# Optimization experiments

Hardware: AMD Instinct MI355X
Metric: run time of the kernel (lower is better)

Reference implementation:

```python
import jax, jax.numpy as jnp
import numpy as np

K = 9          # kernel_size (search window)
PAD = 4        # padding = (K-1)//2

def setup_inputs() -> dict:
    key = jax.random.key(0)
    k1, k2 = jax.random.split(key)
    B, C, H, W = 16, 512, 38, 68
    feat1 = jax.random.normal(k1, (B, C, H, W), dtype=jnp.float32)
    feat2 = jax.random.normal(k2, (B, C, H, W), dtype=jnp.float32)
    return {"feat1": feat1, "feat2": feat2}

def reference(feat1, feat2):
    # corr[b,c,k,h,w] = feat1[b,c,h,w] * feat2_pad[b,c,h+dy,w+dx]; output = max over the
    # K*K window offsets k. We compute the max incrementally over the 81 fixed offsets
    # instead of materializing the [B,C,81,H,W] unfold tensor (same math, less memory).
    B, C, H, W = feat1.shape
    f2 = jnp.pad(feat2, ((0, 0), (0, 0), (PAD, PAD), (PAD, PAD)))
    out = None
    for dy in range(K):
        for dx in range(K):
            corr = feat1 * f2[:, :, dy:dy + H, dx:dx + W]  # [B,C,H,W]
            out = corr if out is None else jnp.maximum(out, corr)
    return out
```

## Files before the change

kernel.cpp:

```cpp
#include <hip/hip_runtime.h>


#define BB 16
#define CC 512
#define HH 38
#define WW 68
#define PLANE (HH * WW)
#define S2S 84
#define HMROWS 48

__global__ __launch_bounds__(256) void corr_winmax_kernel(
    const float* __restrict__ f1, const float* __restrict__ f2,
    float* __restrict__ out)
{
    __shared__ float  s2[HH * S2S];
    __shared__ float2 hm[HMROWS * WW];

    const int t = threadIdx.x;
    const int base = blockIdx.x * PLANE;

    for (int i = t; i < 456; i += 256) {
        int r = i / 12, j = i % 12;
        int col = (j < 4) ? j : (j + 68);
        s2[r * S2S + col] = 0.0f;
    }
    for (int i = t; i < 680; i += 256) {
        int rr = i / 68, col = i % 68;
        int row = (rr < 4) ? rr : (rr + 38);
        hm[row * WW + col] = make_float2(0.0f, 0.0f);
    }
    for (int j = t; j < 646; j += 256) {
        int r = j / 17, q = j % 17;
        float4 v = *reinterpret_cast<const float4*>(f2 + base + r * WW + q * 4);
        *reinterpret_cast<float4*>(&s2[r * S2S + 4 + q * 4]) = v;
    }
    __syncthreads();

    for (int j = t; j < 304; j += 256) {
        int r = j >> 3, seg = j & 7, c0 = seg * 9;
        float v[17];
        #pragma unroll
        for (int i = 0; i < 17; ++i) v[i] = s2[r * S2S + c0 + i];
        float ax[16], an[16];
        #pragma unroll
        for (int i = 0; i < 16; ++i) { ax[i] = fmaxf(v[i], v[i+1]); an[i] = fminf(v[i], v[i+1]); }
        float bx[14], bn[14];
        #pragma unroll
        for (int i = 0; i < 14; ++i) { bx[i] = fmaxf(ax[i], ax[i+2]); bn[i] = fminf(an[i], an[i+2]); }
        float cx[10], cn[10];
        #pragma unroll
        for (int i = 0; i < 10; ++i) { cx[i] = fmaxf(bx[i], bx[i+4]); cn[i] = fminf(bn[i], bn[i+4]); }
        #pragma unroll
        for (int k = 0; k < 9; ++k) {
            int col = c0 + k;
            if (col < WW)
                hm[(r + 4) * WW + col] =
                    make_float2(fmaxf(cx[k], v[k+8]), fminf(cn[k], v[k+8]));
        }
    }
    __syncthreads();

    for (int j = t; j < 272; j += 256) {
        int col = j % 68, vs = j / 68, h0 = vs * 10;
        float2 u[18];
        #pragma unroll
        for (int i = 0; i < 18; ++i) u[i] = hm[(h0 + i) * WW + col];
        float ax[17], an[17];
        #pragma unroll
        for (int i = 0; i < 17; ++i) { ax[i] = fmaxf(u[i].x, u[i+1].x); an[i] = fminf(u[i].y, u[i+1].y); }
        float bx[15], bn[15];
        #pragma unroll
        for (int i = 0; i < 15; ++i) { bx[i] = fmaxf(ax[i], ax[i+2]); bn[i] = fminf(an[i], an[i+2]); }
        float cx[11], cn[11];
        #pragma unroll
        for (int i = 0; i < 11; ++i) { cx[i] = fmaxf(bx[i], bx[i+4]); cn[i] = fminf(bn[i], bn[i+4]); }
        #pragma unroll
        for (int k = 0; k < 10; ++k) {
            int h = h0 + k;
            if (h < HH) {
                float mx = fmaxf(cx[k], u[k+8].x);
                float mn = fminf(cn[k], u[k+8].y);
                int idx = base + h * WW + col;
                float a = f1[idx];
                out[idx] = a * (a >= 0.0f ? mx : mn);
            }
        }
    }
}

extern "C" void kernel_launch(void* const* d_in, const int* in_sizes, int n_in,
                              void* d_out, int out_size, void* d_ws, size_t ws_size,
                              hipStream_t stream) {
    const float* f1 = (const float*)d_in[0];
    const float* f2 = (const float*)d_in[1];
    float* out = (float*)d_out;
    corr_winmax_kernel<<<dim3(BB * CC), dim3(256), 0, stream>>>(f1, f2, out);
}
```

Measured before the change: 51.25 us.

## Split max/min passes to shrink shared memory and raise occupancy

The separable window max/min is restructured into two sequential passes, max then min, that share a single float horizontal buffer instead of a float2 buffer. The staging copy of feat2 into shared memory is dropped, and feat2 is read straight from global with boundary checks. Blocks grow to 320 threads with a launch bound of 8 blocks per CU, and the vertical pass handles two columns per thread with float2 loads and stores. This cuts shared memory and register pressure to allow more resident blocks, at the cost of reading feat2 from global twice, an extra barrier pair, and poorly coalesced scalar global loads.

Result: slower. 75.01 us (+46.4%).

```diff
diff --git a/kernel.cpp b/kernel.cpp
--- a/kernel.cpp
+++ b/kernel.cpp
@@ -1,89 +1,125 @@
 #include <hip/hip_runtime.h>
 
 
-#define BB 16
-#define CC 512
 #define HH 38
 #define WW 68
 #define PLANE (HH * WW)
-#define S2S 84
-#define HMROWS 48
+#define NB (16 * 512)
+#define HBR 46
+#define TPB 320
 
-__global__ __launch_bounds__(256) void corr_winmax_kernel(
+__global__ __launch_bounds__(TPB, 8) void corr_sep_kernel(
     const float* __restrict__ f1, const float* __restrict__ f2,
     float* __restrict__ out)
 {
-    __shared__ float  s2[HH * S2S];
-    __shared__ float2 hm[HMROWS * WW];
+    __shared__ float hbuf[HBR * WW];
+    __shared__ float vmax[HH * WW];
 
     const int t = threadIdx.x;
     const int base = blockIdx.x * PLANE;
+    const float* __restrict__ f2p = f2 + base;
 
-    for (int i = t; i < 456; i += 256) {
-        int r = i / 12, j = i % 12;
-        int col = (j < 4) ? j : (j + 68);
-        s2[r * S2S + col] = 0.0f;
+    for (int i = t; i < 136; i += TPB) {
+        int rr = i / 17, q = i % 17;
+        int row = (rr < 4) ? rr : rr + HH;
+        *reinterpret_cast<float4*>(&hbuf[row * WW + q * 4]) = make_float4(0, 0, 0, 0);
     }
-    for (int i = t; i < 680; i += 256) {
-        int rr = i / 68, col = i % 68;
-        int row = (rr < 4) ? rr : (rr + 38);
-        hm[row * WW + col] = make_float2(0.0f, 0.0f);
-    }
-    for (int j = t; j < 646; j += 256) {
-        int r = j / 17, q = j % 17;
-        float4 v = *reinterpret_cast<const float4*>(f2 + base + r * WW + q * 4);
-        *reinterpret_cast<float4*>(&s2[r * S2S + 4 + q * 4]) = v;
-    }
-    __syncthreads();
 
-    for (int j = t; j < 304; j += 256) {
-        int r = j >> 3, seg = j & 7, c0 = seg * 9;
+    if (t < 304) {
+        int r = t >> 3, seg = t & 7, c0 = seg * 9;
         float v[17];
         #pragma unroll
-        for (int i = 0; i < 17; ++i) v[i] = s2[r * S2S + c0 + i];
-        float ax[16], an[16];
+        for (int i = 0; i < 17; ++i) {
+            int cc = c0 - 4 + i;
+            v[i] = (cc >= 0 && cc < WW) ? f2p[r * WW + cc] : 0.0f;
+        }
+        float d1[16], d2[14], d4[10];
         #pragma unroll
-        for (int i = 0; i < 16; ++i) { ax[i] = fmaxf(v[i], v[i+1]); an[i] = fminf(v[i], v[i+1]); }
-        float bx[14], bn[14];
+        for (int i = 0; i < 16; ++i) d1[i] = fmaxf(v[i], v[i + 1]);
         #pragma unroll
-        for (int i = 0; i < 14; ++i) { bx[i] = fmaxf(ax[i], ax[i+2]); bn[i] = fminf(an[i], an[i+2]); }
-        float cx[10], cn[10];
+        for (int i = 0; i < 14; ++i) d2[i] = fmaxf(d1[i], d1[i + 2]);
         #pragma unroll
-        for (int i = 0; i < 10; ++i) { cx[i] = fmaxf(bx[i], bx[i+4]); cn[i] = fminf(bn[i], bn[i+4]); }
+        for (int i = 0; i < 10; ++i) d4[i] = fmaxf(d2[i], d2[i + 4]);
         #pragma unroll
         for (int k = 0; k < 9; ++k) {
             int col = c0 + k;
-            if (col < WW)
-                hm[(r + 4) * WW + col] =
-                    make_float2(fmaxf(cx[k], v[k+8]), fminf(cn[k], v[k+8]));
+            if (col < WW) hbuf[(r + 4) * WW + col] = fmaxf(d4[k], v[k + 8]);
         }
     }
     __syncthreads();
 
-    for (int j = t; j < 272; j += 256) {
-        int col = j % 68, vs = j / 68, h0 = vs * 10;
+    if (t < 136) {
+        int cp = t % 34, vs = t / 34;
+        int c2 = cp * 2;
+        int h0 = (vs == 3) ? 28 : vs * 10;
         float2 u[18];
         #pragma unroll
-        for (int i = 0; i < 18; ++i) u[i] = hm[(h0 + i) * WW + col];
-        float ax[17], an[17];
+        for (int i = 0; i < 18; ++i)
+            u[i] = *reinterpret_cast<const float2*>(&hbuf[(h0 + i) * WW + c2]);
+        float2 d1[17], d2[15], d4[10];
         #pragma unroll
-        for (int i = 0; i < 17; ++i) { ax[i] = fmaxf(u[i].x, u[i+1].x); an[i] = fminf(u[i].y, u[i+1].y); }
-        float bx[15], bn[15];
+        for (int i = 0; i < 17; ++i) d1[i] = make_float2(fmaxf(u[i].x, u[i+1].x), fmaxf(u[i].y, u[i+1].y));
         #pragma unroll
-        for (int i = 0; i < 15; ++i) { bx[i] = fmaxf(ax[i], ax[i+2]); bn[i] = fminf(an[i], an[i+2]); }
-        float cx[11], cn[11];
+        for (int i = 0; i < 15; ++i) d2[i] = make_float2(fmaxf(d1[i].x, d1[i+2].x), fmaxf(d1[i].y, d1[i+2].y));
         #pragma unroll
-        for (int i = 0; i < 11; ++i) { cx[i] = fmaxf(bx[i], bx[i+4]); cn[i] = fminf(bn[i], bn[i+4]); }
+        for (int i = 0; i < 10; ++i) d4[i] = make_float2(fmaxf(d2[i].x, d2[i+4].x), fmaxf(d2[i].y, d2[i+4].y));
         #pragma unroll
         for (int k = 0; k < 10; ++k) {
             int h = h0 + k;
-            if (h < HH) {
-                float mx = fmaxf(cx[k], u[k+8].x);
-                float mn = fminf(cn[k], u[k+8].y);
-                int idx = base + h * WW + col;
-                float a = f1[idx];
-                out[idx] = a * (a >= 0.0f ? mx : mn);
-            }
+            float2 m = make_float2(fmaxf(d4[k].x, u[k+8].x), fmaxf(d4[k].y, u[k+8].y));
+            *reinterpret_cast<float2*>(&vmax[h * WW + c2]) = m;
+        }
+    }
+    __syncthreads();
+
+    if (t < 304) {
+        int r = t >> 3, seg = t & 7, c0 = seg * 9;
+        float v[17];
+        #pragma unroll
+        for (int i = 0; i < 17; ++i) {
+            int cc = c0 - 4 + i;
+            v[i] = (cc >= 0 && cc < WW) ? f2p[r * WW + cc] : 0.0f;
+        }
+        float d1[16], d2[14], d4[10];
+        #pragma unroll
+        for (int i = 0; i < 16; ++i) d1[i] = fminf(v[i], v[i + 1]);
+        #pragma unroll
+        for (int i = 0; i < 14; ++i) d2[i] = fminf(d1[i], d1[i + 2]);
+        #pragma unroll
+        for (int i = 0; i < 10; ++i) d4[i] = fminf(d2[i], d2[i + 4]);
+        #pragma unroll
+        for (int k = 0; k < 9; ++k) {
+            int col = c0 + k;
+            if (col < WW) hbuf[(r + 4) * WW + col] = fminf(d4[k], v[k + 8]);
+        }
+    }
+    __syncthreads();
+
+    if (t < 136) {
+        int cp = t % 34, vs = t / 34;
+        int c2 = cp * 2;
+        int h0 = (vs == 3) ? 28 : vs * 10;
+        float2 u[18];
+        #pragma unroll
+        for (int i = 0; i < 18; ++i)
+            u[i] = *reinterpret_cast<const float2*>(&hbuf[(h0 + i) * WW + c2]);
+        float2 d1[17], d2[15], d4[10];
+        #pragma unroll
+        for (int i = 0; i < 17; ++i) d1[i] = make_float2(fminf(u[i].x, u[i+1].x), fminf(u[i].y, u[i+1].y));
+        #pragma unroll
+        for (int i = 0; i < 15; ++i) d2[i] = make_float2(fminf(d1[i].x, d1[i+2].x), fminf(d1[i].y, d1[i+2].y));
+        #pragma unroll
+        for (int i = 0; i < 10; ++i) d4[i] = make_float2(fminf(d2[i].x, d2[i+4].x), fminf(d2[i].y, d2[i+4].y));
+        #pragma unroll
+        for (int k = 0; k < 10; ++k) {
+            int h = h0 + k;
+            float2 mn = make_float2(fminf(d4[k].x, u[k+8].x), fminf(d4[k].y, u[k+8].y));
+            float2 mx = *reinterpret_cast<const float2*>(&vmax[h * WW + c2]);
+            float2 a  = *reinterpret_cast<const float2*>(&f1[base + h * WW + c2]);
+            float2 res;
+            res.x = a.x * (a.x >= 0.0f ? mx.x : mn.x);
+            res.y = a.y * (a.y >= 0.0f ? mx.y : mn.y);
+            *reinterpret_cast<float2*>(&out[base + h * WW + c2]) = res;
         }
     }
 }
@@ -94,5 +130,5 @@
     const float* f1 = (const float*)d_in[0];
     const float* f2 = (const float*)d_in[1];
     float* out = (float*)d_out;
-    corr_winmax_kernel<<<dim3(BB * CC), dim3(256), 0, stream>>>(f1, f2, out);
+    corr_sep_kernel<<<dim3(NB), dim3(TPB), 0, stream>>>(f1, f2, out);
 }
```

## Load feat2 directly from global into horizontal pass, drop staging buffer

Applied to the files above, without the earlier changes.

Removes the shared-memory staging buffer for feat2 and its separate zero-padding and copy phase. The horizontal min/max pass now reads global memory directly with bounds checks, which eliminates one barrier and the padded LDS buffer. The block grows to 320 threads so each row segment and column strip gets one thread without loops. The last vertical strip is shifted to overlap the previous one, so its stores need no row guard. In exchange, the scalar global loads are unaligned and overlapping across threads, so they are less coalesced than the earlier float4 copy.

Result: slower. 57.81 us (+12.8%).

```diff
diff --git a/kernel.cpp b/kernel.cpp
--- a/kernel.cpp
+++ b/kernel.cpp
@@ -1,46 +1,37 @@
 #include <hip/hip_runtime.h>
 
 
-#define BB 16
-#define CC 512
 #define HH 38
 #define WW 68
 #define PLANE (HH * WW)
-#define S2S 84
-#define HMROWS 48
+#define NB (16 * 512)
+#define HBR 46
+#define TPB 320
 
-__global__ __launch_bounds__(256) void corr_winmax_kernel(
+__global__ __launch_bounds__(TPB) void corr_fused_kernel(
     const float* __restrict__ f1, const float* __restrict__ f2,
     float* __restrict__ out)
 {
-    __shared__ float  s2[HH * S2S];
-    __shared__ float2 hm[HMROWS * WW];
+    __shared__ float2 hm[HBR * WW];
 
     const int t = threadIdx.x;
     const int base = blockIdx.x * PLANE;
+    const float* __restrict__ f2p = f2 + base;
 
-    for (int i = t; i < 456; i += 256) {
-        int r = i / 12, j = i % 12;
-        int col = (j < 4) ? j : (j + 68);
-        s2[r * S2S + col] = 0.0f;
+    if (t < 272) {
+        int rr = t / 34, q = t % 34;
+        int row = (rr < 4) ? rr : rr + HH;
+        *reinterpret_cast<float4*>(&hm[row * WW + q * 2]) = make_float4(0, 0, 0, 0);
     }
-    for (int i = t; i < 680; i += 256) {
-        int rr = i / 68, col = i % 68;
-        int row = (rr < 4) ? rr : (rr + 38);
-        hm[row * WW + col] = make_float2(0.0f, 0.0f);
-    }
-    for (int j = t; j < 646; j += 256) {
-        int r = j / 17, q = j % 17;
-        float4 v = *reinterpret_cast<const float4*>(f2 + base + r * WW + q * 4);
-        *reinterpret_cast<float4*>(&s2[r * S2S + 4 + q * 4]) = v;
-    }
-    __syncthreads();
 
-    for (int j = t; j < 304; j += 256) {
-        int r = j >> 3, seg = j & 7, c0 = seg * 9;
+    if (t < 304) {
+        int r = t >> 3, seg = t & 7, c0 = seg * 9;
         float v[17];
         #pragma unroll
-        for (int i = 0; i < 17; ++i) v[i] = s2[r * S2S + c0 + i];
+        for (int i = 0; i < 17; ++i) {
+            int cc = c0 - 4 + i;
+            v[i] = (cc >= 0 && cc < WW) ? f2p[r * WW + cc] : 0.0f;
+        }
         float ax[16], an[16];
         #pragma unroll
         for (int i = 0; i < 16; ++i) { ax[i] = fmaxf(v[i], v[i+1]); an[i] = fminf(v[i], v[i+1]); }
@@ -60,8 +51,9 @@
     }
     __syncthreads();
 
-    for (int j = t; j < 272; j += 256) {
-        int col = j % 68, vs = j / 68, h0 = vs * 10;
+    if (t < 272) {
+        int col = t % WW, vs = t / WW;
+        int h0 = (vs == 3) ? 28 : vs * 10;
         float2 u[18];
         #pragma unroll
         for (int i = 0; i < 18; ++i) u[i] = hm[(h0 + i) * WW + col];
@@ -71,19 +63,17 @@
         float bx[15], bn[15];
         #pragma unroll
         for (int i = 0; i < 15; ++i) { bx[i] = fmaxf(ax[i], ax[i+2]); bn[i] = fminf(an[i], an[i+2]); }
-        float cx[11], cn[11];
+        float cx[10], cn[10];
         #pragma unroll
-        for (int i = 0; i < 11; ++i) { cx[i] = fmaxf(bx[i], bx[i+4]); cn[i] = fminf(bn[i], bn[i+4]); }
+        for (int i = 0; i < 10; ++i) { cx[i] = fmaxf(bx[i], bx[i+4]); cn[i] = fminf(bn[i], bn[i+4]); }
         #pragma unroll
         for (int k = 0; k < 10; ++k) {
             int h = h0 + k;
-            if (h < HH) {
-                float mx = fmaxf(cx[k], u[k+8].x);
-                float mn = fminf(cn[k], u[k+8].y);
-                int idx = base + h * WW + col;
-                float a = f1[idx];
-                out[idx] = a * (a >= 0.0f ? mx : mn);
-            }
+            float mx = fmaxf(cx[k], u[k+8].x);
+            float mn = fminf(cn[k], u[k+8].y);
+            int idx = base + h * WW + col;
+            float a = f1[idx];
+            out[idx] = a * (a >= 0.0f ? mx : mn);
         }
     }
 }
@@ -94,5 +84,5 @@
     const float* f1 = (const float*)d_in[0];
     const float* f2 = (const float*)d_in[1];
     float* out = (float*)d_out;
-    corr_winmax_kernel<<<dim3(BB * CC), dim3(256), 0, stream>>>(f1, f2, out);
+    corr_fused_kernel<<<dim3(NB), dim3(TPB), 0, stream>>>(f1, f2, out);
 }
```
